# Optimization experiments

Measured on AMD Instinct MI355X. Metric: run time of the kernel, lower is better.

## Reference

```python
import jax, jax.numpy as jnp
import numpy as np

NUM_HEADS = 16
NUM_UNITS = 1024
NEG = -2.0**32 + 1.0
EPS = 1e-8


def setup_inputs() -> dict:
    key = jax.random.key(0)
    ks = jax.random.split(key, 8)
    B, T, C = 2, 2048, 1024
    U = NUM_UNITS
    x = jax.random.normal(ks[0], (B, T, C), dtype=jnp.float32)
    s = 1.0 / np.sqrt(C)
    Wq = jax.random.normal(ks[1], (C, U), dtype=jnp.float32) * s
    Wk = jax.random.normal(ks[2], (C, U), dtype=jnp.float32) * s
    Wv = jax.random.normal(ks[3], (C, U), dtype=jnp.float32) * s
    bq = jnp.zeros((U,), dtype=jnp.float32)
    bk = jnp.zeros((U,), dtype=jnp.float32)
    bv = jnp.zeros((U,), dtype=jnp.float32)
    gamma = jnp.ones((U,), dtype=jnp.float32)
    beta = jnp.zeros((U,), dtype=jnp.float32)
    return {"x": x, "Wq": Wq, "bq": bq, "Wk": Wk, "bk": bk,
            "Wv": Wv, "bv": bv, "gamma": gamma, "beta": beta}


def _attention(x, Wq, bq, Wk, bk, Wv, bv, gamma, beta):
    B, T, C = x.shape
    H = NUM_HEADS
    U = NUM_UNITS
    dh = U // H
    # Dense projections with relu activation (Keras Dense(activation='relu'))
    Q = jax.nn.relu(x @ Wq + bq)  # [B, T, U]
    K = jax.nn.relu(x @ Wk + bk)
    V = jax.nn.relu(x @ Wv + bv)
    # split into heads: tf.split(axis=2) + concat(axis=0) == [B, T, H, dh]
    Qh = Q.reshape(B, T, H, dh)
    Kh = K.reshape(B, T, H, dh)
    Vh = V.reshape(B, T, H, dh)
    # scaled dot-product scores: scale by sqrt(d_head) (K_ last dim after split)
    scores = jnp.einsum('bqhd,bkhd->bhqk', Qh, Kh) / np.sqrt(dh)
    # key mask: sign(|sum(keys, -1)|) over the ORIGINAL keys input (= x)
    key_mask = jnp.sign(jnp.abs(jnp.sum(x, axis=-1)))  # [B, Tk]
    scores = jnp.where(key_mask[:, None, None, :] == 0, NEG, scores)
    # causal mask (lower-triangular)
    tril = jnp.tril(jnp.ones((T, T), dtype=scores.dtype))
    scores = jnp.where(tril[None, None, :, :] == 0, NEG, scores)
    attn = jax.nn.softmax(scores, axis=-1)
    # query mask: multiply attention rows for zero queries
    query_mask = jnp.sign(jnp.abs(jnp.sum(x, axis=-1)))  # [B, Tq]
    attn = attn * query_mask[:, None, :, None]
    # dropout rate is 0 -> identity
    out = jnp.einsum('bhqk,bkhd->bqhd', attn, Vh).reshape(B, T, U)
    # residual with original queries
    out = out + x
    # layer norm over last axis (tf.nn.moments: biased variance)
    mean = jnp.mean(out, axis=-1, keepdims=True)
    var = jnp.mean((out - mean) ** 2, axis=-1, keepdims=True)
    normalized = (out - mean) / jnp.sqrt(var + EPS)
    return gamma * normalized + beta


def reference(x, Wq, bq, Wk, bk, Wv, bv, gamma, beta):
    return _attention(x, Wq, bq, Wk, bk, Wv, bv, gamma, beta)
```

## Files before the change

### kernel.cpp

```cpp
#include <hip/hip_runtime.h>
#include <math.h>

#define BB 2
#define TT 2048
#define CC 1024
#define UU 1024
#define HH 16
#define DH 64
#define BT (BB*TT)

typedef __attribute__((ext_vector_type(8))) __bf16 bf16x8;
typedef __attribute__((ext_vector_type(4))) __bf16 bf16x4;
typedef __attribute__((ext_vector_type(4))) float f32x4;

#define GLL16(g, l) __builtin_amdgcn_global_load_lds( \
    (__attribute__((address_space(1))) const void*)(g), \
    (__attribute__((address_space(3))) void*)(l), 16, 0, 0)

#define C2EXP 0.18033688011112042f
#define MBIAS 64.0f

__global__ __launch_bounds__(256) void prep_kernel(
    const float* __restrict__ x, float* __restrict__ kadd, __bf16* __restrict__ xb,
    const float* __restrict__ Wq, const float* __restrict__ Wk,
    const float* __restrict__ Wv, __bf16* __restrict__ Wt) {
    const int bx = blockIdx.x;
    const int t = threadIdx.x;
    if (bx < BT) {
        int row = bx;
        float4 v = *(const float4*)&x[(size_t)row * CC + t * 4];
        bf16x4 o;
        o[0] = (__bf16)v.x; o[1] = (__bf16)v.y; o[2] = (__bf16)v.z; o[3] = (__bf16)v.w;
        *(bf16x4*)&xb[(size_t)row * CC + t * 4] = o;
        float s = v.x + v.y + v.z + v.w;
#pragma unroll
        for (int off = 32; off; off >>= 1) s += __shfl_down(s, off, 64);
        __shared__ float red[4];
        int lane = t & 63, w = t >> 6;
        if (lane == 0) red[w] = s;
        __syncthreads();
        if (t == 0) {
            float tot = red[0] + red[1] + red[2] + red[3];
            kadd[row] = (tot == 0.f ? -1.0e30f : 0.f) - MBIAS;
        }
    } else {
        int bz = bx - BT;
        int z = bz >> 8, rem = bz & 255;
        const float* W = z == 0 ? Wq : (z == 1 ? Wk : Wv);
        __bf16* Out = Wt + (size_t)z * CC * UU;
        __shared__ float tile[64][65];
        int n0 = (rem & 15) * 64, k0 = (rem >> 4) * 64;
        int r = t >> 4, c4 = (t & 15) * 4;
#pragma unroll
        for (int i = 0; i < 4; ++i) {
            float4 v = *(const float4*)&W[(size_t)(k0 + r + i * 16) * UU + n0 + c4];
            tile[r + i * 16][c4 + 0] = v.x; tile[r + i * 16][c4 + 1] = v.y;
            tile[r + i * 16][c4 + 2] = v.z; tile[r + i * 16][c4 + 3] = v.w;
        }
        __syncthreads();
#pragma unroll
        for (int i = 0; i < 4; ++i) {
            int nr = r + i * 16;
            bf16x4 o;
            o[0] = (__bf16)tile[c4 + 0][nr]; o[1] = (__bf16)tile[c4 + 1][nr];
            o[2] = (__bf16)tile[c4 + 2][nr]; o[3] = (__bf16)tile[c4 + 3][nr];
            *(bf16x4*)&Out[(size_t)(n0 + nr) * CC + k0 + c4] = o;
        }
    }
}

__global__ __launch_bounds__(256, 4) void qkv_mfma(
    const __bf16* __restrict__ xb, const __bf16* __restrict__ Wt_all,
    const float* __restrict__ bq, const float* __restrict__ bk,
    const float* __restrict__ bv,
    __bf16* __restrict__ Qo, __bf16* __restrict__ Ko, __bf16* __restrict__ VTo) {
    const int z = blockIdx.z;
    const __bf16* Wt = Wt_all + (size_t)z * CC * UU;
    const float* bias = z == 0 ? bq : (z == 1 ? bk : bv);

    const int m0 = blockIdx.x * 128, n0 = blockIdx.y * 128;
    const int t = threadIdx.x, w = t >> 6, lane = t & 63;
    const int quad = lane >> 4, nn = lane & 15;
    const int wr = w >> 1, wc = w & 1;

    __shared__ __bf16 smem[2 * 128 * 64];
    __bf16* As = smem;
    __bf16* Bs = smem + 128 * 64;

    f32x4 acc[4][4];
#pragma unroll
    for (int i = 0; i < 4; ++i)
#pragma unroll
        for (int j = 0; j < 4; ++j) acc[i][j] = (f32x4){0.f, 0.f, 0.f, 0.f};

    for (int k0 = 0; k0 < CC; k0 += 64) {
        __syncthreads();
#pragma unroll
        for (int i = 0; i < 4; ++i) {
            int c = i * 256 + t;
            int row = c >> 3;
            int gc = ((c & 7) ^ (row & 7)) * 8;
            GLL16(&xb[(size_t)(m0 + row) * CC + k0 + gc], &As[c * 8]);
            GLL16(&Wt[(size_t)(n0 + row) * CC + k0 + gc], &Bs[c * 8]);
        }
        __syncthreads();
#pragma unroll
        for (int kk = 0; kk < 2; ++kk) {
            bf16x8 af[4], bfr[4];
#pragma unroll
            for (int i = 0; i < 4; ++i) {
                int R = wr * 64 + i * 16 + nn;
                af[i] = *(const bf16x8*)&As[R * 64 + (((kk * 4 + quad) ^ (R & 7)) * 8)];
            }
#pragma unroll
            for (int j = 0; j < 4; ++j) {
                int R = wc * 64 + j * 16 + nn;
                bfr[j] = *(const bf16x8*)&Bs[R * 64 + (((kk * 4 + quad) ^ (R & 7)) * 8)];
            }
#pragma unroll
            for (int i = 0; i < 4; ++i)
#pragma unroll
                for (int j = 0; j < 4; ++j)
                    acc[i][j] = __builtin_amdgcn_mfma_f32_16x16x32_bf16(af[i], bfr[j], acc[i][j], 0, 0, 0);
        }
    }

    __bf16* cw = &smem[w * 1024];
    float bv4[4];
#pragma unroll
    for (int j = 0; j < 4; ++j) bv4[j] = bias[n0 + wc * 64 + j * 16 + nn];

    __syncthreads();

    if (z < 2) {
        __bf16* Out = z == 0 ? Qo : Ko;
#pragma unroll
        for (int i = 0; i < 4; ++i) {
#pragma unroll
            for (int j = 0; j < 4; ++j)
#pragma unroll
                for (int r = 0; r < 4; ++r)
                    cw[(quad * 4 + r) * 64 + j * 16 + nn] =
                        (__bf16)fmaxf(acc[i][j][r] + bv4[j], 0.f);
            int rr = lane >> 2, cc = (lane & 3) * 16;
            bf16x8 v0 = *(const bf16x8*)&cw[rr * 64 + cc];
            bf16x8 v1 = *(const bf16x8*)&cw[rr * 64 + cc + 8];
            size_t o = (size_t)(m0 + wr * 64 + i * 16 + rr) * UU + n0 + wc * 64 + cc;
            *(bf16x8*)&Out[o] = v0;
            *(bf16x8*)&Out[o + 8] = v1;
        }
    } else {
#pragma unroll
        for (int i = 0; i < 4; ++i) {
#pragma unroll
            for (int j = 0; j < 4; ++j)
#pragma unroll
                for (int r = 0; r < 4; ++r)
                    cw[(j * 16 + nn) * 16 + quad * 4 + r] =
                        (__bf16)fmaxf(acc[i][j][r] + bv4[j], 0.f);
            bf16x8 v0 = *(const bf16x8*)&cw[lane * 16];
            bf16x8 v1 = *(const bf16x8*)&cw[lane * 16 + 8];
            size_t o = (size_t)(n0 + wc * 64 + lane) * BT + m0 + wr * 64 + i * 16;
            *(bf16x8*)&VTo[o] = v0;
            *(bf16x8*)&VTo[o + 8] = v1;
        }
    }
}

__global__ __launch_bounds__(256, 4) void attn_mfma(
    const __bf16* __restrict__ Q, const __bf16* __restrict__ K,
    const __bf16* __restrict__ Vt, const float* __restrict__ kadd,
    __bf16* __restrict__ Obf, float* __restrict__ Op0, float* __restrict__ Op1,
    float* __restrict__ lq0, float* __restrict__ lq1) {
    const int bh = blockIdx.x, b = bh >> 4, h = bh & 15;
    const int cx = blockIdx.y;
    const int p = cx >> 1, half = cx & 1;
    const int col0 = h * 64, rowbase = b * TT;
    const int qa = p, qb = 31 - p;

    const int t = threadIdx.x;
    const int w = t >> 6, lane = t & 63, quad = lane >> 4, nn = lane & 15;
    const int s7 = nn & 7;

    __shared__ __align__(16) __bf16 ks[2][64 * 64];
    __shared__ __align__(16) __bf16 vt[2][64 * 64];
    __shared__ __align__(16) __bf16 ps[64 * 64];

    const int c0 = t;
    const int r0 = c0 >> 3, g0 = ((c0 & 7) ^ (r0 & 7)) * 8;
    const int prow = 16 * w + nn;

    const size_t KSTRIDE = 64 * (size_t)UU;
    const __bf16* kb0 = &K[(size_t)(rowbase + r0) * UU + col0 + g0];
    const __bf16* kb1 = kb0 + 32 * (size_t)UU;
    const __bf16* vb0 = &Vt[(size_t)(col0 + r0) * BT + rowbase + g0];
    const __bf16* vb1 = vb0 + 32 * (size_t)BT;
    const float* kab = &kadd[rowbase + quad * 4];

#define STAGE_TILE(BUF, KP0, KP1, VP0, VP1)   \
    GLL16((KP0), &ks[BUF][c0 * 8]);           \
    GLL16((KP1), &ks[BUF][c0 * 8 + 2048]);    \
    GLL16((VP0), &vt[BUF][c0 * 8]);           \
    GLL16((VP1), &vt[BUF][c0 * 8 + 2048]);

#define LOADKA(KT)                            \
    _Pragma("unroll")                         \
    for (int ct = 0; ct < 4; ++ct)            \
        ka[ct] = *(const f32x4*)&kab[(KT) * 64 + ct * 16];

    float lp = 0.f;
    f32x4 oc[4];
#pragma unroll
    for (int dt = 0; dt < 4; ++dt) oc[dt] = (f32x4){0.f, 0.f, 0.f, 0.f};
    int cur = 0;
    f32x4 ka[4];
    bf16x8 bq0, bq1;

#define ATTN_CORE(KSC, VTC, DIAG)                                              \
  {                                                                            \
    const __bf16* ksc = (KSC);                                                 \
    const __bf16* vtc = (VTC);                                                 \
    _Pragma("unroll")                                                          \
    for (int ct = 0; ct < 4; ++ct) {                                           \
      int krow = ct * 16 + nn;                                                 \
      bf16x8 a0 = *(const bf16x8*)&ksc[krow * 64 + ((quad ^ s7) * 8)];         \
      bf16x8 a1 = *(const bf16x8*)&ksc[krow * 64 + (((4 + quad) ^ s7) * 8)];   \
      f32x4 sc = (f32x4){0.f, 0.f, 0.f, 0.f};                                  \
      __builtin_amdgcn_s_setprio(1);                                           \
      sc = __builtin_amdgcn_mfma_f32_16x16x32_bf16(a0, bq0, sc, 0, 0, 0);      \
      sc = __builtin_amdgcn_mfma_f32_16x16x32_bf16(a1, bq1, sc, 0, 0, 0);      \
      __builtin_amdgcn_s_setprio(0);                                           \
      bf16x4 pw;                                                               \
      _Pragma("unroll")                                                        \
      for (int r = 0; r < 4; ++r) {                                            \
        float arg = fmaf(sc[r], C2EXP, ka[ct][r]);                             \
        if (DIAG) {                                                            \
          int kl = ct * 16 + quad * 4 + r;                                     \
          if (kl > prow) arg = -1.0e30f;                                       \
        }                                                                      \
        float pv = __builtin_amdgcn_exp2f(arg);                                \
        lp += pv;                                                              \
        pw[r] = (__bf16)pv;                                                    \
      }                                                                        \
      int chunk = ct * 2 + (quad >> 1);                                        \
      *(bf16x4*)&ps[prow * 64 + ((chunk ^ s7) * 8) + (quad & 1) * 4] = pw;     \
    }                                                                          \
    bf16x8 bp0 = *(const bf16x8*)&ps[prow * 64 + ((quad ^ s7) * 8)];           \
    bf16x8 bp1 = *(const bf16x8*)&ps[prow * 64 + (((4 + quad) ^ s7) * 8)];     \
    __builtin_amdgcn_s_setprio(1);                                             \
    _Pragma("unroll")                                                          \
    for (int dt = 0; dt < 4; ++dt) {                                           \
      int vrow = dt * 16 + nn;                                                 \
      bf16x8 a0 = *(const bf16x8*)&vtc[vrow * 64 + ((quad ^ s7) * 8)];         \
      bf16x8 a1 = *(const bf16x8*)&vtc[vrow * 64 + (((4 + quad) ^ s7) * 8)];   \
      oc[dt] = __builtin_amdgcn_mfma_f32_16x16x32_bf16(a0, bp0, oc[dt], 0, 0, 0); \
      oc[dt] = __builtin_amdgcn_mfma_f32_16x16x32_bf16(a1, bp1, oc[dt], 0, 0, 0); \
    }                                                                          \
    __builtin_amdgcn_s_setprio(0);                                             \
  }

    if (half == 0) {
        {
            const __bf16* qrow = &Q[(size_t)(rowbase + qa * 64 + prow) * UU + col0];
            bq0 = *(const bf16x8*)&qrow[quad * 8];
            bq1 = *(const bf16x8*)&qrow[32 + quad * 8];
        }
        const __bf16* kp0 = kb0; const __bf16* kp1 = kb1;
        const __bf16* vp0 = vb0; const __bf16* vp1 = vb1;
        STAGE_TILE(0, kp0, kp1, vp0, vp1)
        kp0 += KSTRIDE; kp1 += KSTRIDE; vp0 += 64; vp1 += 64;
        asm volatile("s_waitcnt vmcnt(0)" ::: "memory");
        __builtin_amdgcn_s_barrier();

        for (int kt = 0; kt < qa; ++kt) {
            LOADKA(kt)
            __builtin_amdgcn_sched_barrier(0);
            STAGE_TILE(cur ^ 1, kp0, kp1, vp0, vp1)
            kp0 += KSTRIDE; kp1 += KSTRIDE; vp0 += 64; vp1 += 64;
            __builtin_amdgcn_sched_barrier(0);
            ATTN_CORE(ks[cur], vt[cur], false)
            cur ^= 1;
            asm volatile("s_waitcnt vmcnt(0)" ::: "memory");
            __builtin_amdgcn_s_barrier();
        }
        {
            LOADKA(qa)
            __builtin_amdgcn_sched_barrier(0);
            STAGE_TILE(cur ^ 1, kb0, kb1, vb0, vb1)
            __builtin_amdgcn_sched_barrier(0);
            ATTN_CORE(ks[cur], vt[cur], true)
            cur ^= 1;
            asm volatile("s_waitcnt vmcnt(0)" ::: "memory");
            __builtin_amdgcn_s_barrier();
        }
        {
            float l = lp;
            l += __shfl_xor(l, 16, 64);
            l += __shfl_xor(l, 32, 64);
            const int grow = rowbase + qa * 64 + prow;
            float qsel = (kadd[grow] < -1.0e29f) ? 0.f : 1.f;
            float mult = qsel / fmaxf(l, 1e-37f);
#pragma unroll
            for (int dt = 0; dt < 4; ++dt) {
                bf16x4 ov;
                ov[0] = (__bf16)(oc[dt][0] * mult); ov[1] = (__bf16)(oc[dt][1] * mult);
                ov[2] = (__bf16)(oc[dt][2] * mult); ov[3] = (__bf16)(oc[dt][3] * mult);
                *(bf16x4*)&Obf[(size_t)grow * UU + col0 + dt * 16 + quad * 4] = ov;
            }
        }
        lp = 0.f;
#pragma unroll
        for (int dt = 0; dt < 4; ++dt) oc[dt] = (f32x4){0.f, 0.f, 0.f, 0.f};
        {
            const __bf16* qrow = &Q[(size_t)(rowbase + qb * 64 + prow) * UU + col0];
            bq0 = *(const bf16x8*)&qrow[quad * 8];
            bq1 = *(const bf16x8*)&qrow[32 + quad * 8];
        }
        kp0 = kb0 + KSTRIDE; kp1 = kb1 + KSTRIDE;
        vp0 = vb0; vp1 = vb1;
        const int nb = 16 - p;
        for (int kt = 0; kt < nb - 1; ++kt) {
            LOADKA(kt)
            __builtin_amdgcn_sched_barrier(0);
            STAGE_TILE(cur ^ 1, kp0, kp1, vp0, vp1)
            kp0 += KSTRIDE; kp1 += KSTRIDE; vp0 += 64; vp1 += 64;
            __builtin_amdgcn_sched_barrier(0);
            ATTN_CORE(ks[cur], vt[cur], false)
            cur ^= 1;
            asm volatile("s_waitcnt vmcnt(0)" ::: "memory");
            __builtin_amdgcn_s_barrier();
        }
        LOADKA(nb - 1)
        ATTN_CORE(ks[cur], vt[cur], false)
        {
            float l = lp;
            l += __shfl_xor(l, 16, 64);
            l += __shfl_xor(l, 32, 64);
            const int grow = rowbase + qb * 64 + prow;
            if (quad == 0) lq0[(size_t)grow * HH + h] = l;
            size_t orow = (size_t)(grow - (b + 1) * 1024);
#pragma unroll
            for (int dt = 0; dt < 4; ++dt)
                *(f32x4*)&Op0[orow * UU + col0 + dt * 16 + quad * 4] = oc[dt];
        }
    } else {
        const int k0t = 16 - p;
        {
            const __bf16* qrow = &Q[(size_t)(rowbase + qb * 64 + prow) * UU + col0];
            bq0 = *(const bf16x8*)&qrow[quad * 8];
            bq1 = *(const bf16x8*)&qrow[32 + quad * 8];
        }
        const __bf16* kp0 = kb0 + (size_t)k0t * KSTRIDE;
        const __bf16* kp1 = kb1 + (size_t)k0t * KSTRIDE;
        const __bf16* vp0 = vb0 + k0t * 64;
        const __bf16* vp1 = vb1 + k0t * 64;
        STAGE_TILE(0, kp0, kp1, vp0, vp1)
        kp0 += KSTRIDE; kp1 += KSTRIDE; vp0 += 64; vp1 += 64;
        asm volatile("s_waitcnt vmcnt(0)" ::: "memory");
        __builtin_amdgcn_s_barrier();

        for (int i = 0; i < 15; ++i) {
            LOADKA(k0t + i)
            __builtin_amdgcn_sched_barrier(0);
            STAGE_TILE(cur ^ 1, kp0, kp1, vp0, vp1)
            kp0 += KSTRIDE; kp1 += KSTRIDE; vp0 += 64; vp1 += 64;
            __builtin_amdgcn_sched_barrier(0);
            ATTN_CORE(ks[cur], vt[cur], false)
            cur ^= 1;
            asm volatile("s_waitcnt vmcnt(0)" ::: "memory");
            __builtin_amdgcn_s_barrier();
        }
        LOADKA(k0t + 15)
        ATTN_CORE(ks[cur], vt[cur], true)
        {
            float l = lp;
            l += __shfl_xor(l, 16, 64);
            l += __shfl_xor(l, 32, 64);
            const int grow = rowbase + qb * 64 + prow;
            if (quad == 0) lq1[(size_t)grow * HH + h] = l;
            size_t orow = (size_t)(grow - (b + 1) * 1024);
#pragma unroll
            for (int dt = 0; dt < 4; ++dt)
                *(f32x4*)&Op1[orow * UU + col0 + dt * 16 + quad * 4] = oc[dt];
        }
    }
#undef ATTN_CORE
#undef STAGE_TILE
#undef LOADKA
}

__global__ __launch_bounds__(256) void ln_kernel(
    const __bf16* __restrict__ Obf, const float* __restrict__ Op0,
    const float* __restrict__ Op1, const float* __restrict__ lq0,
    const float* __restrict__ lq1, const float* __restrict__ kadd,
    const float* __restrict__ x, const float* __restrict__ gamma,
    const float* __restrict__ beta, float* __restrict__ out) {
    int row = blockIdx.x;
    int b = row >> 11;
    int qt = (row & (TT - 1)) >> 6;
    size_t base = (size_t)row * UU;
    int t = threadIdx.x;
    float v0, v1, v2, v3;
    float4 xv = *(const float4*)&x[base + t * 4];
    if (qt < 16) {
        bf16x4 ov = *(const bf16x4*)&Obf[base + t * 4];
        v0 = (float)ov[0] + xv.x; v1 = (float)ov[1] + xv.y;
        v2 = (float)ov[2] + xv.z; v3 = (float)ov[3] + xv.w;
    } else {
        int h = t >> 4;
        float l = lq0[(size_t)row * HH + h] + lq1[(size_t)row * HH + h];
        size_t base1 = (size_t)(row - (b + 1) * 1024) * UU;
        f32x4 o0 = *(const f32x4*)&Op0[base1 + t * 4];
        f32x4 o1 = *(const f32x4*)&Op1[base1 + t * 4];
        float qsel = (kadd[row] < -1.0e29f) ? 0.f : 1.f;
        float mult = qsel / fmaxf(l, 1e-37f);
        v0 = (o0[0] + o1[0]) * mult + xv.x; v1 = (o0[1] + o1[1]) * mult + xv.y;
        v2 = (o0[2] + o1[2]) * mult + xv.z; v3 = (o0[3] + o1[3]) * mult + xv.w;
    }
    float s1 = v0 + v1 + v2 + v3;
    float s2 = v0 * v0 + v1 * v1 + v2 * v2 + v3 * v3;
#pragma unroll
    for (int off = 32; off; off >>= 1) {
        s1 += __shfl_down(s1, off, 64);
        s2 += __shfl_down(s2, off, 64);
    }
    __shared__ float r1[4], r2[4];
    int lane = t & 63, w = t >> 6;
    if (lane == 0) { r1[w] = s1; r2[w] = s2; }
    __syncthreads();
    s1 = r1[0] + r1[1] + r1[2] + r1[3];
    s2 = r2[0] + r2[1] + r2[2] + r2[3];
    float mean = s1 * (1.0f / 1024.0f);
    float var = s2 * (1.0f / 1024.0f) - mean * mean;
    float rstd = rsqrtf(var + 1e-8f);
    float4 g = *(const float4*)&gamma[t * 4];
    float4 be = *(const float4*)&beta[t * 4];
    float4 ores;
    ores.x = g.x * (v0 - mean) * rstd + be.x;
    ores.y = g.y * (v1 - mean) * rstd + be.y;
    ores.z = g.z * (v2 - mean) * rstd + be.z;
    ores.w = g.w * (v3 - mean) * rstd + be.w;
    *(float4*)&out[base + t * 4] = ores;
}

extern "C" void kernel_launch(void* const* d_in, const int* in_sizes, int n_in,
                              void* d_out, int out_size, void* d_ws, size_t ws_size,
                              hipStream_t stream) {
    const float* x     = (const float*)d_in[0];
    const float* Wq    = (const float*)d_in[1];
    const float* bq    = (const float*)d_in[2];
    const float* Wk    = (const float*)d_in[3];
    const float* bk    = (const float*)d_in[4];
    const float* Wv    = (const float*)d_in[5];
    const float* bv    = (const float*)d_in[6];
    const float* gamma = (const float*)d_in[7];
    const float* beta  = (const float*)d_in[8];
    float* out = (float*)d_out;

    char* wsb = (char*)d_ws;
    const size_t MB = 1024ull * 1024;
    __bf16* xb  = (__bf16*)(wsb);
    __bf16* Wt  = (__bf16*)(wsb + 8 * MB);
    __bf16* Obf = (__bf16*)(wsb);
    float* Op0  = (float*)(wsb + 8 * MB);
    __bf16* Qb  = (__bf16*)(wsb + 16 * MB);
    __bf16* Kb  = (__bf16*)(wsb + 24 * MB);
    __bf16* Vt  = (__bf16*)(wsb + 32 * MB);
    float* kadd = (float*)(wsb + 40 * MB);
    float* Op1  = (float*)(wsb + 41 * MB);
    float* lq0  = (float*)(wsb + 49 * MB);
    float* lq1  = (float*)(wsb + 50 * MB);

    prep_kernel<<<dim3(BT + 768), dim3(256), 0, stream>>>(x, kadd, xb, Wq, Wk, Wv, Wt);
    qkv_mfma<<<dim3(BT / 128, UU / 128, 3), dim3(256), 0, stream>>>(
        xb, Wt, bq, bk, bv, Qb, Kb, Vt);
    attn_mfma<<<dim3(BB * HH, 32), dim3(256), 0, stream>>>(
        Qb, Kb, Vt, kadd, Obf, Op0, Op1, lq0, lq1);
    ln_kernel<<<dim3(BT), dim3(256), 0, stream>>>(
        Obf, Op0, Op1, lq0, lq1, kadd, x, gamma, beta, out);
}
```

Measured before the change: 165.6 us.

## Switch attention core to 32x32x16 MFMA with 2x2 wave tiling

Replaces the 16x16x32 MFMA attention core, where each wave owned 16 query rows, with 32x32x16 MFMAs on a 2x2 wave grid. Each wave now computes a 32-key by 32-query score block and a 32-dim by 32-query output block, sharing P through LDS across waves. The aim is fewer LDS fragment loads per FLOP and higher MFMA efficiency. In exchange it adds an extra barrier between the QK and PV phases and a cross-wave LDS reduction for the row sums, and it raises accumulator register pressure under the 4-block occupancy bound.

```diff
diff --git a/kernel.cpp b/kernel.cpp
--- a/kernel.cpp
+++ b/kernel.cpp
@@ -12,6 +12,7 @@
 typedef __attribute__((ext_vector_type(8))) __bf16 bf16x8;
 typedef __attribute__((ext_vector_type(4))) __bf16 bf16x4;
 typedef __attribute__((ext_vector_type(4))) float f32x4;
+typedef __attribute__((ext_vector_type(16))) float f32x16;
 
 #define GLL16(g, l) __builtin_amdgcn_global_load_lds( \
     (__attribute__((address_space(1))) const void*)(g), \
@@ -19,6 +20,13 @@
 
 #define C2EXP 0.18033688011112042f
 #define MBIAS 64.0f
+
+__device__ inline f32x16 zero16() {
+    f32x16 z;
+#pragma unroll
+    for (int i = 0; i < 16; ++i) z[i] = 0.f;
+    return z;
+}
 
 __global__ __launch_bounds__(256) void prep_kernel(
     const float* __restrict__ x, float* __restrict__ kadd, __bf16* __restrict__ xb,
@@ -179,8 +187,12 @@
     const int qa = p, qb = 31 - p;
 
     const int t = threadIdx.x;
-    const int w = t >> 6, lane = t & 63, quad = lane >> 4, nn = lane & 15;
-    const int s7 = nn & 7;
+    const int w = t >> 6, lane = t & 63;
+    const int col = lane & 31, hi = lane >> 5;
+    const int wr = w >> 1, wc = w & 1;
+    const int cs7 = col & 7;
+    const int arow = 32 * wr + col;
+    const int qrow = 32 * wc + col;
 
     __shared__ __align__(16) __bf16 ks[2][64 * 64];
     __shared__ __align__(16) __bf16 vt[2][64 * 64];
@@ -188,14 +200,13 @@
 
     const int c0 = t;
     const int r0 = c0 >> 3, g0 = ((c0 & 7) ^ (r0 & 7)) * 8;
-    const int prow = 16 * w + nn;
 
     const size_t KSTRIDE = 64 * (size_t)UU;
     const __bf16* kb0 = &K[(size_t)(rowbase + r0) * UU + col0 + g0];
     const __bf16* kb1 = kb0 + 32 * (size_t)UU;
     const __bf16* vb0 = &Vt[(size_t)(col0 + r0) * BT + rowbase + g0];
     const __bf16* vb1 = vb0 + 32 * (size_t)BT;
-    const float* kab = &kadd[rowbase + quad * 4];
+    const float* kab = &kadd[rowbase + 32 * wr + 4 * hi];
 
 #define STAGE_TILE(BUF, KP0, KP1, VP0, VP1)   \
     GLL16((KP0), &ks[BUF][c0 * 8]);           \
@@ -205,66 +216,105 @@
 
 #define LOADKA(KT)                            \
     _Pragma("unroll")                         \
-    for (int ct = 0; ct < 4; ++ct)            \
-        ka[ct] = *(const f32x4*)&kab[(KT) * 64 + ct * 16];
+    for (int g = 0; g < 4; ++g)               \
+        ka[g] = *(const f32x4*)&kab[(KT) * 64 + g * 8];
+
+#define LOADBQ(Q0)                                                             \
+    {                                                                          \
+        const __bf16* qrp = &Q[(size_t)(rowbase + (Q0) + qrow) * UU + col0];   \
+        _Pragma("unroll")                                                      \
+        for (int ds = 0; ds < 4; ++ds)                                         \
+            bq[ds] = *(const bf16x8*)&qrp[ds * 16 + hi * 8];                   \
+    }
 
     float lp = 0.f;
-    f32x4 oc[4];
-#pragma unroll
-    for (int dt = 0; dt < 4; ++dt) oc[dt] = (f32x4){0.f, 0.f, 0.f, 0.f};
+    f32x16 oc = zero16();
     int cur = 0;
     f32x4 ka[4];
-    bf16x8 bq0, bq1;
-
-#define ATTN_CORE(KSC, VTC, DIAG)                                              \
+    bf16x8 bq[4];
+
+#define ATTN_QK(DIAG)                                                          \
   {                                                                            \
-    const __bf16* ksc = (KSC);                                                 \
-    const __bf16* vtc = (VTC);                                                 \
+    const __bf16* ksc = ks[cur];                                               \
+    f32x16 sc = zero16();                                                      \
+    __builtin_amdgcn_s_setprio(1);                                             \
     _Pragma("unroll")                                                          \
-    for (int ct = 0; ct < 4; ++ct) {                                           \
-      int krow = ct * 16 + nn;                                                 \
-      bf16x8 a0 = *(const bf16x8*)&ksc[krow * 64 + ((quad ^ s7) * 8)];         \
-      bf16x8 a1 = *(const bf16x8*)&ksc[krow * 64 + (((4 + quad) ^ s7) * 8)];   \
-      f32x4 sc = (f32x4){0.f, 0.f, 0.f, 0.f};                                  \
-      __builtin_amdgcn_s_setprio(1);                                           \
-      sc = __builtin_amdgcn_mfma_f32_16x16x32_bf16(a0, bq0, sc, 0, 0, 0);      \
-      sc = __builtin_amdgcn_mfma_f32_16x16x32_bf16(a1, bq1, sc, 0, 0, 0);      \
-      __builtin_amdgcn_s_setprio(0);                                           \
+    for (int ds = 0; ds < 4; ++ds) {                                           \
+      bf16x8 a = *(const bf16x8*)&ksc[arow * 64 + (((ds * 2 + hi) ^ cs7) * 8)];\
+      sc = __builtin_amdgcn_mfma_f32_32x32x16_bf16(a, bq[ds], sc, 0, 0, 0);    \
+    }                                                                          \
+    __builtin_amdgcn_s_setprio(0);                                             \
+    _Pragma("unroll")                                                          \
+    for (int g = 0; g < 4; ++g) {                                              \
       bf16x4 pw;                                                               \
       _Pragma("unroll")                                                        \
-      for (int r = 0; r < 4; ++r) {                                            \
-        float arg = fmaf(sc[r], C2EXP, ka[ct][r]);                             \
+      for (int e = 0; e < 4; ++e) {                                            \
+        float arg = fmaf(sc[g * 4 + e], C2EXP, ka[g][e]);                      \
         if (DIAG) {                                                            \
-          int kl = ct * 16 + quad * 4 + r;                                     \
-          if (kl > prow) arg = -1.0e30f;                                       \
+          int keyl = 32 * wr + 8 * g + 4 * hi + e;                             \
+          if (keyl > qrow) arg = -1.0e30f;                                     \
         }                                                                      \
         float pv = __builtin_amdgcn_exp2f(arg);                                \
         lp += pv;                                                              \
-        pw[r] = (__bf16)pv;                                                    \
+        pw[e] = (__bf16)pv;                                                    \
       }                                                                        \
-      int chunk = ct * 2 + (quad >> 1);                                        \
-      *(bf16x4*)&ps[prow * 64 + ((chunk ^ s7) * 8) + (quad & 1) * 4] = pw;     \
+      *(bf16x4*)&ps[qrow * 64 + (((4 * wr + g) ^ cs7) * 8) + 4 * hi] = pw;     \
     }                                                                          \
-    bf16x8 bp0 = *(const bf16x8*)&ps[prow * 64 + ((quad ^ s7) * 8)];           \
-    bf16x8 bp1 = *(const bf16x8*)&ps[prow * 64 + (((4 + quad) ^ s7) * 8)];     \
+  }
+
+#define ATTN_PV                                                                \
+  {                                                                            \
+    const __bf16* vtc = vt[cur];                                               \
     __builtin_amdgcn_s_setprio(1);                                             \
     _Pragma("unroll")                                                          \
-    for (int dt = 0; dt < 4; ++dt) {                                           \
-      int vrow = dt * 16 + nn;                                                 \
-      bf16x8 a0 = *(const bf16x8*)&vtc[vrow * 64 + ((quad ^ s7) * 8)];         \
-      bf16x8 a1 = *(const bf16x8*)&vtc[vrow * 64 + (((4 + quad) ^ s7) * 8)];   \
-      oc[dt] = __builtin_amdgcn_mfma_f32_16x16x32_bf16(a0, bp0, oc[dt], 0, 0, 0); \
-      oc[dt] = __builtin_amdgcn_mfma_f32_16x16x32_bf16(a1, bp1, oc[dt], 0, 0, 0); \
+    for (int kst = 0; kst < 4; ++kst) {                                        \
+      bf16x8 a = *(const bf16x8*)&vtc[arow * 64 + (((kst * 2 + hi) ^ cs7) * 8)]; \
+      bf16x8 bp = *(const bf16x8*)&ps[qrow * 64 + (((kst * 2 + hi) ^ cs7) * 8)]; \
+      oc = __builtin_amdgcn_mfma_f32_32x32x16_bf16(a, bp, oc, 0, 0, 0);        \
     }                                                                          \
     __builtin_amdgcn_s_setprio(0);                                             \
   }
 
+#define FULL_ITER(KT, KN0, KN1, VN0, VN1, DIAG)                                \
+  {                                                                            \
+    LOADKA(KT)                                                                 \
+    __builtin_amdgcn_sched_barrier(0);                                         \
+    STAGE_TILE(cur ^ 1, KN0, KN1, VN0, VN1)                                    \
+    __builtin_amdgcn_sched_barrier(0);                                         \
+    ATTN_QK(DIAG)                                                              \
+    asm volatile("s_waitcnt lgkmcnt(0)" ::: "memory");                         \
+    __builtin_amdgcn_s_barrier();                                              \
+    __builtin_amdgcn_sched_barrier(0);                                         \
+    ATTN_PV                                                                    \
+    asm volatile("s_waitcnt vmcnt(0)" ::: "memory");                           \
+    __builtin_amdgcn_s_barrier();                                              \
+    cur ^= 1;                                                                  \
+  }
+
+#define LAST_ITER(KT, DIAG)                                                    \
+  {                                                                            \
+    LOADKA(KT)                                                                 \
+    ATTN_QK(DIAG)                                                              \
+    asm volatile("s_waitcnt lgkmcnt(0)" ::: "memory");                         \
+    __builtin_amdgcn_s_barrier();                                              \
+    __builtin_amdgcn_sched_barrier(0);                                         \
+    ATTN_PV                                                                    \
+    __builtin_amdgcn_s_barrier();                                              \
+  }
+
+#define REDUCE_L(LOUT)                                                         \
+    float LOUT;                                                                \
+    {                                                                          \
+        float l2 = lp + __shfl_xor(lp, 32, 64);                                \
+        float* lred = (float*)ps;                                              \
+        if (hi == 0) lred[wc * 64 + wr * 32 + col] = l2;                       \
+        asm volatile("s_waitcnt lgkmcnt(0)" ::: "memory");                     \
+        __builtin_amdgcn_s_barrier();                                          \
+        LOUT = lred[wc * 64 + col] + lred[wc * 64 + 32 + col];                 \
+    }
+
     if (half == 0) {
-        {
-            const __bf16* qrow = &Q[(size_t)(rowbase + qa * 64 + prow) * UU + col0];
-            bq0 = *(const bf16x8*)&qrow[quad * 8];
-            bq1 = *(const bf16x8*)&qrow[32 + quad * 8];
-        }
+        LOADBQ(qa * 64)
         const __bf16* kp0 = kb0; const __bf16* kp1 = kb1;
         const __bf16* vp0 = vb0; const __bf16* vp1 = vb1;
         STAGE_TILE(0, kp0, kp1, vp0, vp1)
@@ -273,83 +323,52 @@
         __builtin_amdgcn_s_barrier();
 
         for (int kt = 0; kt < qa; ++kt) {
-            LOADKA(kt)
-            __builtin_amdgcn_sched_barrier(0);
-            STAGE_TILE(cur ^ 1, kp0, kp1, vp0, vp1)
+            FULL_ITER(kt, kp0, kp1, vp0, vp1, false)
             kp0 += KSTRIDE; kp1 += KSTRIDE; vp0 += 64; vp1 += 64;
-            __builtin_amdgcn_sched_barrier(0);
-            ATTN_CORE(ks[cur], vt[cur], false)
-            cur ^= 1;
-            asm volatile("s_waitcnt vmcnt(0)" ::: "memory");
-            __builtin_amdgcn_s_barrier();
-        }
+        }
+        FULL_ITER(qa, kb0, kb1, vb0, vb1, true)
         {
-            LOADKA(qa)
-            __builtin_amdgcn_sched_barrier(0);
-            STAGE_TILE(cur ^ 1, kb0, kb1, vb0, vb1)
-            __builtin_amdgcn_sched_barrier(0);
-            ATTN_CORE(ks[cur], vt[cur], true)
-            cur ^= 1;
-            asm volatile("s_waitcnt vmcnt(0)" ::: "memory");
-            __builtin_amdgcn_s_barrier();
-        }
-        {
-            float l = lp;
-            l += __shfl_xor(l, 16, 64);
-            l += __shfl_xor(l, 32, 64);
-            const int grow = rowbase + qa * 64 + prow;
+            REDUCE_L(l)
+            const int grow = rowbase + qa * 64 + qrow;
             float qsel = (kadd[grow] < -1.0e29f) ? 0.f : 1.f;
             float mult = qsel / fmaxf(l, 1e-37f);
 #pragma unroll
-            for (int dt = 0; dt < 4; ++dt) {
+            for (int g = 0; g < 4; ++g) {
                 bf16x4 ov;
-                ov[0] = (__bf16)(oc[dt][0] * mult); ov[1] = (__bf16)(oc[dt][1] * mult);
-                ov[2] = (__bf16)(oc[dt][2] * mult); ov[3] = (__bf16)(oc[dt][3] * mult);
-                *(bf16x4*)&Obf[(size_t)grow * UU + col0 + dt * 16 + quad * 4] = ov;
+#pragma unroll
+                for (int e = 0; e < 4; ++e) ov[e] = (__bf16)(oc[g * 4 + e] * mult);
+                *(bf16x4*)&Obf[(size_t)grow * UU + col0 + 32 * wr + 8 * g + 4 * hi] = ov;
             }
+            if (wr == 0 && hi == 0) {  }
+            __builtin_amdgcn_s_barrier();
         }
         lp = 0.f;
-#pragma unroll
-        for (int dt = 0; dt < 4; ++dt) oc[dt] = (f32x4){0.f, 0.f, 0.f, 0.f};
-        {
-            const __bf16* qrow = &Q[(size_t)(rowbase + qb * 64 + prow) * UU + col0];
-            bq0 = *(const bf16x8*)&qrow[quad * 8];
-            bq1 = *(const bf16x8*)&qrow[32 + quad * 8];
-        }
+        oc = zero16();
+        LOADBQ(qb * 64)
         kp0 = kb0 + KSTRIDE; kp1 = kb1 + KSTRIDE;
         vp0 = vb0; vp1 = vb1;
         const int nb = 16 - p;
         for (int kt = 0; kt < nb - 1; ++kt) {
-            LOADKA(kt)
-            __builtin_amdgcn_sched_barrier(0);
-            STAGE_TILE(cur ^ 1, kp0, kp1, vp0, vp1)
+            FULL_ITER(kt, kp0, kp1, vp0, vp1, false)
             kp0 += KSTRIDE; kp1 += KSTRIDE; vp0 += 64; vp1 += 64;
-            __builtin_amdgcn_sched_barrier(0);
-            ATTN_CORE(ks[cur], vt[cur], false)
-            cur ^= 1;
-            asm volatile("s_waitcnt vmcnt(0)" ::: "memory");
-            __builtin_amdgcn_s_barrier();
-        }
-        LOADKA(nb - 1)
-        ATTN_CORE(ks[cur], vt[cur], false)
+        }
+        LAST_ITER(nb - 1, false)
         {
-            float l = lp;
-            l += __shfl_xor(l, 16, 64);
-            l += __shfl_xor(l, 32, 64);
-            const int grow = rowbase + qb * 64 + prow;
-            if (quad == 0) lq0[(size_t)grow * HH + h] = l;
+            REDUCE_L(l)
+            const int grow = rowbase + qb * 64 + qrow;
+            if (wr == 0 && hi == 0) lq0[(size_t)grow * HH + h] = l;
             size_t orow = (size_t)(grow - (b + 1) * 1024);
 #pragma unroll
-            for (int dt = 0; dt < 4; ++dt)
-                *(f32x4*)&Op0[orow * UU + col0 + dt * 16 + quad * 4] = oc[dt];
+            for (int g = 0; g < 4; ++g) {
+                f32x4 ov;
+#pragma unroll
+                for (int e = 0; e < 4; ++e) ov[e] = oc[g * 4 + e];
+                *(f32x4*)&Op0[orow * UU + col0 + 32 * wr + 8 * g + 4 * hi] = ov;
+            }
         }
     } else {
         const int k0t = 16 - p;
-        {
-            const __bf16* qrow = &Q[(size_t)(rowbase + qb * 64 + prow) * UU + col0];
-            bq0 = *(const bf16x8*)&qrow[quad * 8];
-            bq1 = *(const bf16x8*)&qrow[32 + quad * 8];
-        }
+        LOADBQ(qb * 64)
         const __bf16* kp0 = kb0 + (size_t)k0t * KSTRIDE;
         const __bf16* kp1 = kb1 + (size_t)k0t * KSTRIDE;
         const __bf16* vp0 = vb0 + k0t * 64;
@@ -360,33 +379,32 @@
         __builtin_amdgcn_s_barrier();
 
         for (int i = 0; i < 15; ++i) {
-            LOADKA(k0t + i)
-            __builtin_amdgcn_sched_barrier(0);
-            STAGE_TILE(cur ^ 1, kp0, kp1, vp0, vp1)
+            FULL_ITER(k0t + i, kp0, kp1, vp0, vp1, false)
             kp0 += KSTRIDE; kp1 += KSTRIDE; vp0 += 64; vp1 += 64;
-            __builtin_amdgcn_sched_barrier(0);
-            ATTN_CORE(ks[cur], vt[cur], false)
-            cur ^= 1;
-            asm volatile("s_waitcnt vmcnt(0)" ::: "memory");
-            __builtin_amdgcn_s_barrier();
-        }
-        LOADKA(k0t + 15)
-        ATTN_CORE(ks[cur], vt[cur], true)
+        }
+        LAST_ITER(k0t + 15, true)
         {
-            float l = lp;
-            l += __shfl_xor(l, 16, 64);
-            l += __shfl_xor(l, 32, 64);
-            const int grow = rowbase + qb * 64 + prow;
-            if (quad == 0) lq1[(size_t)grow * HH + h] = l;
+            REDUCE_L(l)
+            const int grow = rowbase + qb * 64 + qrow;
+            if (wr == 0 && hi == 0) lq1[(size_t)grow * HH + h] = l;
             size_t orow = (size_t)(grow - (b + 1) * 1024);
 #pragma unroll
-            for (int dt = 0; dt < 4; ++dt)
-                *(f32x4*)&Op1[orow * UU + col0 + dt * 16 + quad * 4] = oc[dt];
-        }
-    }
-#undef ATTN_CORE
+            for (int g = 0; g < 4; ++g) {
+                f32x4 ov;
+#pragma unroll
+                for (int e = 0; e < 4; ++e) ov[e] = oc[g * 4 + e];
+                *(f32x4*)&Op1[orow * UU + col0 + 32 * wr + 8 * g + 4 * hi] = ov;
+            }
+        }
+    }
+#undef REDUCE_L
+#undef LAST_ITER
+#undef FULL_ITER
+#undef ATTN_PV
+#undef ATTN_QK
+#undef LOADBQ
+#undef LOADKA
 #undef STAGE_TILE
-#undef LOADKA
 }
 
 __global__ __launch_bounds__(256) void ln_kernel(
```

Result: no change. 165.7 us (+0.0%).

## Share staged K/V tiles between both query blocks in the half-0 attention path

Applied to the files above, without the earlier changes.

The half==0 branch used to run two separate passes over key/value tiles, one for query block qa and one for qb, each restaging the same early K/V tiles into LDS. It now merges them into a single loop over max(nA, nB) tiles, applying both query blocks to each staged tile with separate accumulators. The goal is fewer global-to-LDS loads and barriers. In exchange it doubles the accumulator registers, which may lower occupancy, and it adds per-iteration branches and a DIAG flag that is now a runtime value.

```diff
diff --git a/kernel.cpp b/kernel.cpp
--- a/kernel.cpp
+++ b/kernel.cpp
@@ -208,15 +208,18 @@
     for (int ct = 0; ct < 4; ++ct)            \
         ka[ct] = *(const f32x4*)&kab[(KT) * 64 + ct * 16];
 
-    float lp = 0.f;
-    f32x4 oc[4];
-#pragma unroll
-    for (int dt = 0; dt < 4; ++dt) oc[dt] = (f32x4){0.f, 0.f, 0.f, 0.f};
+    float lpA = 0.f, lpB = 0.f;
+    f32x4 ocA[4], ocB[4];
+#pragma unroll
+    for (int dt = 0; dt < 4; ++dt) {
+        ocA[dt] = (f32x4){0.f, 0.f, 0.f, 0.f};
+        ocB[dt] = (f32x4){0.f, 0.f, 0.f, 0.f};
+    }
     int cur = 0;
     f32x4 ka[4];
-    bf16x8 bq0, bq1;
-
-#define ATTN_CORE(KSC, VTC, DIAG)                                              \
+    bf16x8 bqA0, bqA1, bqB0, bqB1;
+
+#define ATTN_CORE(KSC, VTC, DIAG, BQ0, BQ1, LP, OC)                            \
   {                                                                            \
     const __bf16* ksc = (KSC);                                                 \
     const __bf16* vtc = (VTC);                                                 \
@@ -227,8 +230,8 @@
       bf16x8 a1 = *(const bf16x8*)&ksc[krow * 64 + (((4 + quad) ^ s7) * 8)];   \
       f32x4 sc = (f32x4){0.f, 0.f, 0.f, 0.f};                                  \
       __builtin_amdgcn_s_setprio(1);                                           \
-      sc = __builtin_amdgcn_mfma_f32_16x16x32_bf16(a0, bq0, sc, 0, 0, 0);      \
-      sc = __builtin_amdgcn_mfma_f32_16x16x32_bf16(a1, bq1, sc, 0, 0, 0);      \
+      sc = __builtin_amdgcn_mfma_f32_16x16x32_bf16(a0, (BQ0), sc, 0, 0, 0);    \
+      sc = __builtin_amdgcn_mfma_f32_16x16x32_bf16(a1, (BQ1), sc, 0, 0, 0);    \
       __builtin_amdgcn_s_setprio(0);                                           \
       bf16x4 pw;                                                               \
       _Pragma("unroll")                                                        \
@@ -239,7 +242,7 @@
           if (kl > prow) arg = -1.0e30f;                                       \
         }                                                                      \
         float pv = __builtin_amdgcn_exp2f(arg);                                \
-        lp += pv;                                                              \
+        (LP) += pv;                                                            \
         pw[r] = (__bf16)pv;                                                    \
       }                                                                        \
       int chunk = ct * 2 + (quad >> 1);                                        \
@@ -253,17 +256,22 @@
       int vrow = dt * 16 + nn;                                                 \
       bf16x8 a0 = *(const bf16x8*)&vtc[vrow * 64 + ((quad ^ s7) * 8)];         \
       bf16x8 a1 = *(const bf16x8*)&vtc[vrow * 64 + (((4 + quad) ^ s7) * 8)];   \
-      oc[dt] = __builtin_amdgcn_mfma_f32_16x16x32_bf16(a0, bp0, oc[dt], 0, 0, 0); \
-      oc[dt] = __builtin_amdgcn_mfma_f32_16x16x32_bf16(a1, bp1, oc[dt], 0, 0, 0); \
+      (OC)[dt] = __builtin_amdgcn_mfma_f32_16x16x32_bf16(a0, bp0, (OC)[dt], 0, 0, 0); \
+      (OC)[dt] = __builtin_amdgcn_mfma_f32_16x16x32_bf16(a1, bp1, (OC)[dt], 0, 0, 0); \
     }                                                                          \
     __builtin_amdgcn_s_setprio(0);                                             \
   }
 
     if (half == 0) {
+        const int nA = qa + 1, nB = 16 - p;
+        const int nmax = nA > nB ? nA : nB;
         {
-            const __bf16* qrow = &Q[(size_t)(rowbase + qa * 64 + prow) * UU + col0];
-            bq0 = *(const bf16x8*)&qrow[quad * 8];
-            bq1 = *(const bf16x8*)&qrow[32 + quad * 8];
+            const __bf16* qrp = &Q[(size_t)(rowbase + qa * 64 + prow) * UU + col0];
+            bqA0 = *(const bf16x8*)&qrp[quad * 8];
+            bqA1 = *(const bf16x8*)&qrp[32 + quad * 8];
+            const __bf16* qrq = &Q[(size_t)(rowbase + qb * 64 + prow) * UU + col0];
+            bqB0 = *(const bf16x8*)&qrq[quad * 8];
+            bqB1 = *(const bf16x8*)&qrq[32 + quad * 8];
         }
         const __bf16* kp0 = kb0; const __bf16* kp1 = kb1;
         const __bf16* vp0 = vb0; const __bf16* vp1 = vb1;
@@ -272,29 +280,28 @@
         asm volatile("s_waitcnt vmcnt(0)" ::: "memory");
         __builtin_amdgcn_s_barrier();
 
-        for (int kt = 0; kt < qa; ++kt) {
+        for (int kt = 0; kt < nmax; ++kt) {
             LOADKA(kt)
             __builtin_amdgcn_sched_barrier(0);
-            STAGE_TILE(cur ^ 1, kp0, kp1, vp0, vp1)
-            kp0 += KSTRIDE; kp1 += KSTRIDE; vp0 += 64; vp1 += 64;
+            if (kt + 1 < nmax) {
+                STAGE_TILE(cur ^ 1, kp0, kp1, vp0, vp1)
+                kp0 += KSTRIDE; kp1 += KSTRIDE; vp0 += 64; vp1 += 64;
+            }
             __builtin_amdgcn_sched_barrier(0);
-            ATTN_CORE(ks[cur], vt[cur], false)
+            if (kt < nA) {
+                ATTN_CORE(ks[cur], vt[cur], kt == qa, bqA0, bqA1, lpA, ocA)
+            }
+            if (kt < nB) {
+                ATTN_CORE(ks[cur], vt[cur], false, bqB0, bqB1, lpB, ocB)
+            }
             cur ^= 1;
-            asm volatile("s_waitcnt vmcnt(0)" ::: "memory");
-            __builtin_amdgcn_s_barrier();
+            if (kt + 1 < nmax) {
+                asm volatile("s_waitcnt vmcnt(0)" ::: "memory");
+                __builtin_amdgcn_s_barrier();
+            }
         }
         {
-            LOADKA(qa)
-            __builtin_amdgcn_sched_barrier(0);
-            STAGE_TILE(cur ^ 1, kb0, kb1, vb0, vb1)
-            __builtin_amdgcn_sched_barrier(0);
-            ATTN_CORE(ks[cur], vt[cur], true)
-            cur ^= 1;
-            asm volatile("s_waitcnt vmcnt(0)" ::: "memory");
-            __builtin_amdgcn_s_barrier();
-        }
-        {
-            float l = lp;
+            float l = lpA;
             l += __shfl_xor(l, 16, 64);
             l += __shfl_xor(l, 32, 64);
             const int grow = rowbase + qa * 64 + prow;
@@ -303,37 +310,13 @@
 #pragma unroll
             for (int dt = 0; dt < 4; ++dt) {
                 bf16x4 ov;
-                ov[0] = (__bf16)(oc[dt][0] * mult); ov[1] = (__bf16)(oc[dt][1] * mult);
-                ov[2] = (__bf16)(oc[dt][2] * mult); ov[3] = (__bf16)(oc[dt][3] * mult);
+                ov[0] = (__bf16)(ocA[dt][0] * mult); ov[1] = (__bf16)(ocA[dt][1] * mult);
+                ov[2] = (__bf16)(ocA[dt][2] * mult); ov[3] = (__bf16)(ocA[dt][3] * mult);
                 *(bf16x4*)&Obf[(size_t)grow * UU + col0 + dt * 16 + quad * 4] = ov;
             }
         }
-        lp = 0.f;
-#pragma unroll
-        for (int dt = 0; dt < 4; ++dt) oc[dt] = (f32x4){0.f, 0.f, 0.f, 0.f};
         {
-            const __bf16* qrow = &Q[(size_t)(rowbase + qb * 64 + prow) * UU + col0];
-            bq0 = *(const bf16x8*)&qrow[quad * 8];
-            bq1 = *(const bf16x8*)&qrow[32 + quad * 8];
-        }
-        kp0 = kb0 + KSTRIDE; kp1 = kb1 + KSTRIDE;
-        vp0 = vb0; vp1 = vb1;
-        const int nb = 16 - p;
-        for (int kt = 0; kt < nb - 1; ++kt) {
-            LOADKA(kt)
-            __builtin_amdgcn_sched_barrier(0);
-            STAGE_TILE(cur ^ 1, kp0, kp1, vp0, vp1)
-            kp0 += KSTRIDE; kp1 += KSTRIDE; vp0 += 64; vp1 += 64;
-            __builtin_amdgcn_sched_barrier(0);
-            ATTN_CORE(ks[cur], vt[cur], false)
-            cur ^= 1;
-            asm volatile("s_waitcnt vmcnt(0)" ::: "memory");
-            __builtin_amdgcn_s_barrier();
-        }
-        LOADKA(nb - 1)
-        ATTN_CORE(ks[cur], vt[cur], false)
-        {
-            float l = lp;
+            float l = lpB;
             l += __shfl_xor(l, 16, 64);
             l += __shfl_xor(l, 32, 64);
             const int grow = rowbase + qb * 64 + prow;
@@ -341,14 +324,14 @@
             size_t orow = (size_t)(grow - (b + 1) * 1024);
 #pragma unroll
             for (int dt = 0; dt < 4; ++dt)
-                *(f32x4*)&Op0[orow * UU + col0 + dt * 16 + quad * 4] = oc[dt];
+                *(f32x4*)&Op0[orow * UU + col0 + dt * 16 + quad * 4] = ocB[dt];
         }
     } else {
         const int k0t = 16 - p;
         {
             const __bf16* qrow = &Q[(size_t)(rowbase + qb * 64 + prow) * UU + col0];
-            bq0 = *(const bf16x8*)&qrow[quad * 8];
-            bq1 = *(const bf16x8*)&qrow[32 + quad * 8];
+            bqA0 = *(const bf16x8*)&qrow[quad * 8];
+            bqA1 = *(const bf16x8*)&qrow[32 + quad * 8];
         }
         const __bf16* kp0 = kb0 + (size_t)k0t * KSTRIDE;
         const __bf16* kp1 = kb1 + (size_t)k0t * KSTRIDE;
@@ -365,15 +348,15 @@
             STAGE_TILE(cur ^ 1, kp0, kp1, vp0, vp1)
             kp0 += KSTRIDE; kp1 += KSTRIDE; vp0 += 64; vp1 += 64;
             __builtin_amdgcn_sched_barrier(0);
-            ATTN_CORE(ks[cur], vt[cur], false)
+            ATTN_CORE(ks[cur], vt[cur], false, bqA0, bqA1, lpA, ocA)
             cur ^= 1;
             asm volatile("s_waitcnt vmcnt(0)" ::: "memory");
             __builtin_amdgcn_s_barrier();
         }
         LOADKA(k0t + 15)
-        ATTN_CORE(ks[cur], vt[cur], true)
+        ATTN_CORE(ks[cur], vt[cur], true, bqA0, bqA1, lpA, ocA)
         {
-            float l = lp;
+            float l = lpA;
             l += __shfl_xor(l, 16, 64);
             l += __shfl_xor(l, 32, 64);
             const int grow = rowbase + qb * 64 + prow;
@@ -381,7 +364,7 @@
             size_t orow = (size_t)(grow - (b + 1) * 1024);
 #pragma unroll
             for (int dt = 0; dt < 4; ++dt)
-                *(f32x4*)&Op1[orow * UU + col0 + dt * 16 + quad * 4] = oc[dt];
+                *(f32x4*)&Op1[orow * UU + col0 + dt * 16 + quad * 4] = ocA[dt];
         }
     }
 #undef ATTN_CORE
```

Result: no change. 165.8 us (+0.1%).
